# Kernel tuning notes

Hardware: AMD Instinct MI355X
Metric: run time of the kernel (lower is better)

## Reference

```python
import jax, jax.numpy as jnp
import numpy as np

B, N_PER, C, KG, KTOP, KNN = 8, 2048, 256, 16, 512, 32
N = B * N_PER
E = N * KG
EPS = 1e-5


def setup_inputs() -> dict:
    key = jax.random.key(0)
    ks = jax.random.split(key, 32)
    s = 0.05
    x = jax.random.normal(ks[0], (N, C), jnp.float32)
    x_origin = jax.random.normal(ks[1], (N, C), jnp.float32)
    xyz = jax.random.uniform(ks[2], (N, 3), jnp.float32)
    # graph: every node is a dst with KG incoming edges from random nodes of the SAME sample
    edge_dst = jnp.repeat(jnp.arange(N, dtype=jnp.int32), KG)
    src_local = jax.random.randint(ks[3], (E,), 0, N_PER, dtype=jnp.int32)
    edge_src = src_local + (edge_dst // N_PER) * N_PER
    # EdgeConv params (theta on x_j - x_i, phi on x_i)
    theta_w = jax.random.normal(ks[4], (C, C), jnp.float32) * s
    theta_b = jax.random.normal(ks[5], (C,), jnp.float32) * s
    phi_w = jax.random.normal(ks[6], (C, C), jnp.float32) * s
    phi_b = jax.random.normal(ks[7], (C,), jnp.float32) * s
    # region_score_mlp: Conv1d(C,64,1)-ReLU-BN(64)-Conv1d(64,32,1)-ReLU-BN(32)-Conv1d(32,1,1)
    w1 = jax.random.normal(ks[8], (64, C), jnp.float32) * s
    b1 = jax.random.normal(ks[9], (64,), jnp.float32) * s
    g1 = 1.0 + 0.1 * jax.random.normal(ks[10], (64,), jnp.float32)
    be1 = 0.1 * jax.random.normal(ks[11], (64,), jnp.float32)
    m1 = 0.1 * jax.random.normal(ks[12], (64,), jnp.float32)
    v1 = jax.random.uniform(ks[13], (64,), jnp.float32, 0.5, 1.5)
    w2 = jax.random.normal(ks[14], (32, 64), jnp.float32) * s
    b2 = jax.random.normal(ks[15], (32,), jnp.float32) * s
    g2 = 1.0 + 0.1 * jax.random.normal(ks[16], (32,), jnp.float32)
    be2 = 0.1 * jax.random.normal(ks[17], (32,), jnp.float32)
    m2 = 0.1 * jax.random.normal(ks[18], (32,), jnp.float32)
    v2 = jax.random.uniform(ks[19], (32,), jnp.float32, 0.5, 1.5)
    w3 = jax.random.normal(ks[20], (1, 32), jnp.float32) * s
    b3 = jax.random.normal(ks[21], (1,), jnp.float32) * s
    return dict(x=x, x_origin=x_origin, xyz=xyz, edge_src=edge_src, edge_dst=edge_dst,
                theta_w=theta_w, theta_b=theta_b, phi_w=phi_w, phi_b=phi_b,
                w1=w1, b1=b1, g1=g1, be1=be1, m1=m1, v1=v1,
                w2=w2, b2=b2, g2=g2, be2=be2, m2=m2, v2=v2, w3=w3, b3=b3)


def _bn(t, g, b, m, v):
    return (t - m) * jax.lax.rsqrt(v + EPS) * g + b


def _forward(x, x_origin, xyz, edge_src, edge_dst,
             theta_w, theta_b, phi_w, phi_b,
             w1, b1, g1, be1, m1, v1, w2, b2, g2, be2, m2, v2, w3, b3):
    # EdgeConv: h_i = max_{j->i}( theta(x_j - x_i) + phi(x_i) ), then residual add
    msg = ((x[edge_src] - x[edge_dst]) @ theta_w.T + theta_b
           + x[edge_dst] @ phi_w.T + phi_b)                      # [E, C]
    h = jax.ops.segment_max(msg, edge_dst, num_segments=N)       # [N, C]
    x1 = h + x                                                   # residual
    # per-node MLP (Conv1d kernel-size 1 == linear), BN in eval mode
    t = _bn(jax.nn.relu(x1 @ w1.T + b1), g1, be1, m1, v1)
    t = _bn(jax.nn.relu(t @ w2.T + b2), g2, be2, m2, v2)
    score = t @ w3.T + b3                                        # [N, 1]
    score_b = score.reshape(B, N_PER)                            # vps_score
    # per-batch top-k (cls=False path: select by raw score, descending)
    topk_vals, topk_idx = jax.lax.top_k(score_b, KTOP)           # [B, KTOP]
    perm = (topk_idx + jnp.arange(B, dtype=topk_idx.dtype)[:, None] * N_PER).reshape(-1)
    x_new = x1[perm].reshape(B, KTOP, C)
    x_copy = x_origin[perm].reshape(B, KTOP, -1)
    xyz_sel = xyz[perm].reshape(B, KTOP, 3)
    # rebuild 32-NN graph per sample on selected points (batched, no per-b python calls)
    d2 = jnp.sum((xyz_sel[:, :, None, :] - xyz_sel[:, None, :, :]) ** 2, axis=-1)  # [B,K,K]
    _, knn_idx = jax.lax.top_k(-d2, KNN)                         # [B, KTOP, 32]
    return knn_idx, x_new, x_copy, score_b, topk_vals


def reference(x, x_origin, xyz, edge_src, edge_dst,
              theta_w, theta_b, phi_w, phi_b,
              w1, b1, g1, be1, m1, v1, w2, b2, g2, be2, m2, v2, w3, b3):
    return _forward(x, x_origin, xyz, edge_src, edge_dst,
                    theta_w, theta_b, phi_w, phi_b,
                    w1, b1, g1, be1, m1, v1, w2, b2, g2, be2, m2, v2, w3, b3)
```

## Files before the change

### kernel.cpp

```cpp
#include <hip/hip_runtime.h>
#include <math.h>

constexpr int B     = 8;
constexpr int N_PER = 2048;
constexpr int C     = 256;
constexpr int KG    = 16;
constexpr int KTOP  = 512;
constexpr int KNN   = 32;
constexpr int N     = B * N_PER;
constexpr float EPS = 1e-5f;

__global__ __launch_bounds__(256, 2) void k1_dual_gemm(
    const float* __restrict__ x, const float* __restrict__ thw,
    const float* __restrict__ phw, const float* __restrict__ thb,
    const float* __restrict__ phb, float* __restrict__ T, float* __restrict__ R)
{
    constexpr int BK = 16, STX = 132, STW = 68;
    __shared__ float Xs[2][BK * STX];
    __shared__ float Wt[2][BK * STW];
    __shared__ float Wp[2][BK * STW];
    const int tid  = threadIdx.x;
    const int row0 = blockIdx.x * 128;
    const int n0   = blockIdx.y * 64;
    const int tx = tid & 15, ty = tid >> 4;
    const int lm = tid >> 1, lq = (tid & 1) * 8;
    const int wm = tid >> 2, wq = (tid & 3) * 4;

    float aT[8][4] = {{0.f}}, aQ[8][4] = {{0.f}};

    float4 nx0 = *(const float4*)(x   + (size_t)(row0 + lm) * C + lq);
    float4 nx1 = *(const float4*)(x   + (size_t)(row0 + lm) * C + lq + 4);
    float4 nt  = *(const float4*)(thw + (size_t)(n0   + wm) * C + wq);
    float4 np_ = *(const float4*)(phw + (size_t)(n0   + wm) * C + wq);
    Xs[0][(lq + 0) * STX + lm] = nx0.x;  Xs[0][(lq + 1) * STX + lm] = nx0.y;
    Xs[0][(lq + 2) * STX + lm] = nx0.z;  Xs[0][(lq + 3) * STX + lm] = nx0.w;
    Xs[0][(lq + 4) * STX + lm] = nx1.x;  Xs[0][(lq + 5) * STX + lm] = nx1.y;
    Xs[0][(lq + 6) * STX + lm] = nx1.z;  Xs[0][(lq + 7) * STX + lm] = nx1.w;
    Wt[0][(wq + 0) * STW + wm] = nt.x;   Wt[0][(wq + 1) * STW + wm] = nt.y;
    Wt[0][(wq + 2) * STW + wm] = nt.z;   Wt[0][(wq + 3) * STW + wm] = nt.w;
    Wp[0][(wq + 0) * STW + wm] = np_.x;  Wp[0][(wq + 1) * STW + wm] = np_.y;
    Wp[0][(wq + 2) * STW + wm] = np_.z;  Wp[0][(wq + 3) * STW + wm] = np_.w;
    __syncthreads();

    int p = 0;
    for (int k0 = 0; k0 < C; k0 += BK) {
        const int kn = k0 + BK;
        if (kn < C) {
            nx0 = *(const float4*)(x   + (size_t)(row0 + lm) * C + kn + lq);
            nx1 = *(const float4*)(x   + (size_t)(row0 + lm) * C + kn + lq + 4);
            nt  = *(const float4*)(thw + (size_t)(n0   + wm) * C + kn + wq);
            np_ = *(const float4*)(phw + (size_t)(n0   + wm) * C + kn + wq);
        }
        const float* Xp = Xs[p];
        const float* Tp = Wt[p];
        const float* Pp = Wp[p];
#pragma unroll
        for (int k = 0; k < BK; ++k) {
            float4 alo = *(const float4*)&Xp[k * STX + ty * 8];
            float4 ahi = *(const float4*)&Xp[k * STX + ty * 8 + 4];
            float4 tv4 = *(const float4*)&Tp[k * STW + tx * 4];
            float4 pv4 = *(const float4*)&Pp[k * STW + tx * 4];
            float av[8] = {alo.x, alo.y, alo.z, alo.w, ahi.x, ahi.y, ahi.z, ahi.w};
            float tv[4] = {tv4.x, tv4.y, tv4.z, tv4.w};
            float pv[4] = {pv4.x, pv4.y, pv4.z, pv4.w};
#pragma unroll
            for (int i2 = 0; i2 < 8; ++i2)
#pragma unroll
                for (int j2 = 0; j2 < 4; ++j2) {
                    aT[i2][j2] += av[i2] * tv[j2];
                    aQ[i2][j2] += av[i2] * pv[j2];
                }
        }
        if (kn < C) {
            const int q = p ^ 1;
            Xs[q][(lq + 0) * STX + lm] = nx0.x;  Xs[q][(lq + 1) * STX + lm] = nx0.y;
            Xs[q][(lq + 2) * STX + lm] = nx0.z;  Xs[q][(lq + 3) * STX + lm] = nx0.w;
            Xs[q][(lq + 4) * STX + lm] = nx1.x;  Xs[q][(lq + 5) * STX + lm] = nx1.y;
            Xs[q][(lq + 6) * STX + lm] = nx1.z;  Xs[q][(lq + 7) * STX + lm] = nx1.w;
            Wt[q][(wq + 0) * STW + wm] = nt.x;   Wt[q][(wq + 1) * STW + wm] = nt.y;
            Wt[q][(wq + 2) * STW + wm] = nt.z;   Wt[q][(wq + 3) * STW + wm] = nt.w;
            Wp[q][(wq + 0) * STW + wm] = np_.x;  Wp[q][(wq + 1) * STW + wm] = np_.y;
            Wp[q][(wq + 2) * STW + wm] = np_.z;  Wp[q][(wq + 3) * STW + wm] = np_.w;
            __syncthreads();
        }
        p ^= 1;
    }

    const int gn = n0 + tx * 4;
    const float4 tb4 = *(const float4*)(thb + gn);
    const float4 pb4 = *(const float4*)(phb + gn);
#pragma unroll
    for (int i2 = 0; i2 < 8; ++i2) {
        const int gm = row0 + ty * 8 + i2;
        const size_t off = (size_t)gm * C + gn;
        float4 xr = *(const float4*)(x + off);
        float4 tvv = make_float4(aT[i2][0], aT[i2][1], aT[i2][2], aT[i2][3]);
        float4 rv;
        rv.x = xr.x + aQ[i2][0] + tb4.x + pb4.x - tvv.x;
        rv.y = xr.y + aQ[i2][1] + tb4.y + pb4.y - tvv.y;
        rv.z = xr.z + aQ[i2][2] + tb4.z + pb4.z - tvv.z;
        rv.w = xr.w + aQ[i2][3] + tb4.w + pb4.w - tvv.w;
        *(float4*)(T + off) = tvv;
        *(float4*)(R + off) = rv;
    }
}

__global__ __launch_bounds__(256) void k2a_gather_max(
    const int* __restrict__ esrc, const float* __restrict__ T, float* x1r)
{
    const int gb = blockIdx.x;
    const int b  = gb & 7;
    const int node0 = b * N_PER + (gb >> 3) * 4;
    const int t = threadIdx.x;
    __shared__ int s[4][KG];
    if (t < 64) s[t >> 4][t & 15] = esrc[(node0 + (t >> 4)) * KG + (t & 15)];
    __syncthreads();
    const int m  = t >> 6;
    const int c4 = (t & 63) * 4;
    float4 acc = make_float4(-INFINITY, -INFINITY, -INFINITY, -INFINITY);
#pragma unroll
    for (int k = 0; k < KG; ++k) {
        const float4 v = *(const float4*)&T[(size_t)s[m][k] * C + c4];
        acc.x = fmaxf(acc.x, v.x);  acc.y = fmaxf(acc.y, v.y);
        acc.z = fmaxf(acc.z, v.z);  acc.w = fmaxf(acc.w, v.w);
    }
    const size_t off = (size_t)(node0 + m) * C + c4;
    float4 r = *(const float4*)&x1r[off];
    r.x += acc.x;  r.y += acc.y;  r.z += acc.z;  r.w += acc.w;
    *(float4*)&x1r[off] = r;
}

__global__ __launch_bounds__(256) void k2bc_score(
    const float* __restrict__ x1, const float* __restrict__ w1,
    const float* __restrict__ b1, const float* __restrict__ g1,
    const float* __restrict__ be1, const float* __restrict__ m1,
    const float* __restrict__ v1,
    const float* __restrict__ w2, const float* __restrict__ b2,
    const float* __restrict__ g2, const float* __restrict__ be2,
    const float* __restrict__ m2, const float* __restrict__ v2,
    const float* __restrict__ w3, const float* __restrict__ b3,
    float* __restrict__ score_ws, float* __restrict__ out_score)
{
    constexpr int BK = 16, ST = 68;
    __shared__ float Xs[BK * ST];
    __shared__ float Ws[BK * ST];
    __shared__ float t1s[64 * 65];
    __shared__ float w2s[32 * 65];
    __shared__ float w3s[32];
    __shared__ float zs[64 * 33];
    const int tid  = threadIdx.x;
    const int row0 = blockIdx.x * 64;
    const int tx = tid & 15, ty = tid >> 4;
    const int lm = tid >> 2, lq = (tid & 3) << 2;

    float acc[4][4] = {{0.f}};
    for (int k0 = 0; k0 < C; k0 += BK) {
        float4 fx = *(const float4*)(x1 + (size_t)(row0 + lm) * C + k0 + lq);
        float4 fw = *(const float4*)(w1 + (size_t)lm * C + k0 + lq);
        __syncthreads();
        Xs[(lq + 0) * ST + lm] = fx.x;  Xs[(lq + 1) * ST + lm] = fx.y;
        Xs[(lq + 2) * ST + lm] = fx.z;  Xs[(lq + 3) * ST + lm] = fx.w;
        Ws[(lq + 0) * ST + lm] = fw.x;  Ws[(lq + 1) * ST + lm] = fw.y;
        Ws[(lq + 2) * ST + lm] = fw.z;  Ws[(lq + 3) * ST + lm] = fw.w;
        __syncthreads();
#pragma unroll
        for (int k = 0; k < BK; ++k) {
            float4 a4 = *(const float4*)&Xs[k * ST + (ty << 2)];
            float4 w4 = *(const float4*)&Ws[k * ST + (tx << 2)];
            float av[4] = {a4.x, a4.y, a4.z, a4.w};
            float wv[4] = {w4.x, w4.y, w4.z, w4.w};
#pragma unroll
            for (int i2 = 0; i2 < 4; ++i2)
#pragma unroll
                for (int j2 = 0; j2 < 4; ++j2) acc[i2][j2] += av[i2] * wv[j2];
        }
    }
    __syncthreads();
#pragma unroll
    for (int i2 = 0; i2 < 4; ++i2) {
        const int mrow = (ty << 2) + i2;
#pragma unroll
        for (int j2 = 0; j2 < 4; ++j2) {
            const int o = (tx << 2) + j2;
            float y = acc[i2][j2] + b1[o];
            y = fmaxf(y, 0.f);
            y = (y - m1[o]) * (1.0f / sqrtf(v1[o] + EPS)) * g1[o] + be1[o];
            t1s[mrow * 65 + o] = y;
        }
    }
    for (int idx = tid; idx < 2048; idx += 256)
        w2s[(idx >> 6) * 65 + (idx & 63)] = w2[idx];
    if (tid < 32) w3s[tid] = w3[tid];
    __syncthreads();

    const int o = tid & 31;
    const float inv2 = (1.0f / sqrtf(v2[o] + EPS)) * g2[o];
#pragma unroll
    for (int p = 0; p < 8; ++p) {
        const int nl = p * 8 + (tid >> 5);
        float z = 0.f;
#pragma unroll
        for (int j = 0; j < 64; ++j) z += t1s[nl * 65 + j] * w2s[o * 65 + j];
        z += b2[o];
        z = fmaxf(z, 0.f);
        z = (z - m2[o]) * inv2 + be2[o];
        zs[nl * 33 + o] = z;
    }
    __syncthreads();

    if (tid < 64) {
        float sacc = 0.f;
#pragma unroll
        for (int j = 0; j < 32; ++j) sacc += zs[tid * 33 + j] * w3s[j];
        sacc += b3[0];
        const int node = row0 + tid;
        score_ws[node]  = sacc;
        out_score[node] = sacc;
    }
}

__global__ __launch_bounds__(1024) void k3_topk(
    const float* __restrict__ score, const float* __restrict__ xyz,
    float* __restrict__ out_topk, int* __restrict__ perm,
    float* __restrict__ xsel)
{
    __shared__ unsigned long long keys[N_PER];
    const int b = blockIdx.x;
    const int t = threadIdx.x;
    for (int i = t; i < N_PER; i += 1024) {
        const float v = score[b * N_PER + i];
        unsigned u = __float_as_uint(v);
        const unsigned ua = (u & 0x80000000u) ? ~u : (u | 0x80000000u);
        const unsigned ud = ~ua;
        keys[i] = ((unsigned long long)ud << 32) | (unsigned)i;
    }
    __syncthreads();
    for (int k = 2; k <= N_PER; k <<= 1) {
        for (int j = k >> 1; j > 0; j >>= 1) {
            for (int i = t; i < N_PER; i += 1024) {
                const int ixj = i ^ j;
                if (ixj > i) {
                    const unsigned long long a = keys[i], c = keys[ixj];
                    const bool up = ((i & k) == 0);
                    if ((a > c) == up) { keys[i] = c; keys[ixj] = a; }
                }
            }
            __syncthreads();
        }
    }
    for (int r = t; r < KTOP; r += 1024) {
        const int idx = (int)(keys[r] & 0xffffffffu);
        const int g = b * N_PER + idx;
        out_topk[b * KTOP + r] = score[g];
        perm[b * KTOP + r] = g;
        xsel[(b * KTOP + r) * 3 + 0] = xyz[g * 3 + 0];
        xsel[(b * KTOP + r) * 3 + 1] = xyz[g * 3 + 1];
        xsel[(b * KTOP + r) * 3 + 2] = xyz[g * 3 + 2];
    }
}

__global__ __launch_bounds__(256) void k5_knn(
    const int* __restrict__ perm, const float* __restrict__ xsel,
    const float* __restrict__ x1, const float* __restrict__ xorig,
    float* __restrict__ out_xnew, float* __restrict__ out_xcopy,
    float* __restrict__ out_knn)
{
    constexpr int G = 4;
    __shared__ float px[KTOP], py[KTOP], pz[KTOP];
    __shared__ unsigned long long keys[G * KTOP];
    const int t  = threadIdx.x;
    const int q0 = blockIdx.x * G;
    const int b  = q0 >> 9;
    const int i0 = q0 & 511;

    for (int idx = t; idx < KTOP; idx += 256) {
        const size_t base = ((size_t)b * KTOP + idx) * 3;
        px[idx] = xsel[base + 0];
        py[idx] = xsel[base + 1];
        pz[idx] = xsel[base + 2];
    }
#pragma unroll
    for (int p = 0; p < G; ++p) {
        const int row = q0 + p;
        const int g = perm[row];
        out_xnew [(size_t)row * C + t] = x1   [(size_t)g * C + t];
        out_xcopy[(size_t)row * C + t] = xorig[(size_t)g * C + t];
    }
    __syncthreads();

    for (int w = t; w < G * KTOP; w += 256) {
        const int p = w >> 9, idx = w & 511;
        const float dx = __fsub_rn(px[i0 + p], px[idx]);
        const float dy = __fsub_rn(py[i0 + p], py[idx]);
        const float dz = __fsub_rn(pz[i0 + p], pz[idx]);
        const float d2 = __fadd_rn(__fadd_rn(__fmul_rn(dx, dx), __fmul_rn(dy, dy)),
                                   __fmul_rn(dz, dz));
        keys[w] = ((unsigned long long)__float_as_uint(d2) << 32) | (unsigned)idx;
    }
    __syncthreads();

    for (int k = 2; k <= 32; k <<= 1) {
        for (int j = k >> 1; j > 0; j >>= 1) {
            for (int i = t; i < G * KTOP; i += 256) {
                const int ixj = i ^ j;
                if (ixj > i) {
                    const int il = i & 31;
                    const unsigned long long a = keys[i], c = keys[ixj];
                    const bool up = ((il & k) == 0) || (k == 32);
                    if ((a > c) == up) { keys[i] = c; keys[ixj] = a; }
                }
            }
            __syncthreads();
        }
    }
    for (int r = 0; r < 4; ++r) {
        const int npairs = 8 >> r;
        const int total  = G * npairs * 32;
        for (int w = t; w < total; w += 256) {
            const int p  = w / (npairs * 32);
            const int rm = w - p * (npairs * 32);
            const int m  = rm >> 5, i = rm & 31;
            const int baseA = p * KTOP + m * (64 << r);
            const int baseB = baseA + (32 << r);
            const unsigned long long a = keys[baseA + i];
            const unsigned long long c = keys[baseB + 31 - i];
            keys[baseA + i] = (c < a) ? c : a;
        }
        __syncthreads();
        for (int j = 16; j > 0; j >>= 1) {
            for (int w = t; w < total; w += 256) {
                const int p  = w / (npairs * 32);
                const int rm = w - p * (npairs * 32);
                const int m  = rm >> 5, i = rm & 31;
                const int ixj = i ^ j;
                if (ixj > i) {
                    const int baseA = p * KTOP + m * (64 << r);
                    const unsigned long long a = keys[baseA + i], c = keys[baseA + ixj];
                    if (a > c) { keys[baseA + i] = c; keys[baseA + ixj] = a; }
                }
            }
            __syncthreads();
        }
    }

    if (t < G * KNN) {
        const int p = t >> 5, r = t & 31;
        out_knn[((size_t)(q0 + p)) * KNN + r] =
            (float)(unsigned)(keys[p * KTOP + r] & 0xffffffffu);
    }
}

extern "C" void kernel_launch(void* const* d_in, const int* in_sizes, int n_in,
                              void* d_out, int out_size, void* d_ws, size_t ws_size,
                              hipStream_t stream)
{
    const float* x     = (const float*)d_in[0];
    const float* xorig = (const float*)d_in[1];
    const float* xyz   = (const float*)d_in[2];
    const int*   esrc  = (const int*)d_in[3];
    const float* thw = (const float*)d_in[5];
    const float* thb = (const float*)d_in[6];
    const float* phw = (const float*)d_in[7];
    const float* phb = (const float*)d_in[8];
    const float* w1  = (const float*)d_in[9];
    const float* b1  = (const float*)d_in[10];
    const float* g1  = (const float*)d_in[11];
    const float* be1 = (const float*)d_in[12];
    const float* m1  = (const float*)d_in[13];
    const float* v1  = (const float*)d_in[14];
    const float* w2  = (const float*)d_in[15];
    const float* b2  = (const float*)d_in[16];
    const float* g2  = (const float*)d_in[17];
    const float* be2 = (const float*)d_in[18];
    const float* m2  = (const float*)d_in[19];
    const float* v2  = (const float*)d_in[20];
    const float* w3  = (const float*)d_in[21];
    const float* b3  = (const float*)d_in[22];

    float* ws   = (float*)d_ws;
    float* T    = ws;
    float* x1   = ws + (size_t)N * C;
    float* sc   = ws + 2 * (size_t)N * C;
    int*   perm = (int*)(sc + N);
    float* xsel = (float*)(perm + B * KTOP);

    float* out     = (float*)d_out;
    float* o_knn   = out;
    float* o_xnew  = o_knn + (size_t)B * KTOP * KNN;
    float* o_xcopy = o_xnew + (size_t)B * KTOP * C;
    float* o_score = o_xcopy + (size_t)B * KTOP * C;
    float* o_topk  = o_score + (size_t)B * N_PER;

    k1_dual_gemm<<<dim3(N / 128, C / 64), 256, 0, stream>>>(x, thw, phw, thb, phb, T, x1);
    k2a_gather_max<<<N / 4, 256, 0, stream>>>(esrc, T, x1);
    k2bc_score<<<N / 64, 256, 0, stream>>>(x1, w1, b1, g1, be1, m1, v1,
                                           w2, b2, g2, be2, m2, v2, w3, b3, sc, o_score);
    k3_topk<<<B, 1024, 0, stream>>>(sc, xyz, o_topk, perm, xsel);
    k5_knn<<<B * KTOP / 4, 256, 0, stream>>>(perm, xsel, x1, xorig,
                                             o_xnew, o_xcopy, o_knn);
}
```

Measured before the change: 266.5 us.

## Widen GEMM K-tile, hold w2 in registers, and double k5 queries per block

The dual GEMM K-tile goes from 16 to 32, so each thread loads more per stage and the kernel hits half as many barriers, at the cost of more shared memory and registers per block. The score kernel now keeps its w2 row in registers and reads t1 with float4 loads, which drops the w2 shared buffer. The kNN kernel handles 8 query rows per block instead of 4 and copies the gathered rows with float4 loads and stores. The larger shared footprint in k1 and k5 may lower occupancy.

New measurement: 308.4 us. +15.7%, slower.

```diff
diff --git a/kernel.cpp b/kernel.cpp
--- a/kernel.cpp
+++ b/kernel.cpp
@@ -15,7 +15,7 @@
     const float* __restrict__ phw, const float* __restrict__ thb,
     const float* __restrict__ phb, float* __restrict__ T, float* __restrict__ R)
 {
-    constexpr int BK = 16, STX = 132, STW = 68;
+    constexpr int BK = 32, STX = 132, STW = 68;
     __shared__ float Xs[2][BK * STX];
     __shared__ float Wt[2][BK * STW];
     __shared__ float Wp[2][BK * STW];
@@ -23,33 +23,47 @@
     const int row0 = blockIdx.x * 128;
     const int n0   = blockIdx.y * 64;
     const int tx = tid & 15, ty = tid >> 4;
-    const int lm = tid >> 1, lq = (tid & 1) * 8;
-    const int wm = tid >> 2, wq = (tid & 3) * 4;
+    const int lm = tid >> 1, lq = (tid & 1) * 16;
+    const int wm = tid >> 2, wq = (tid & 3) * 8;
 
     float aT[8][4] = {{0.f}}, aQ[8][4] = {{0.f}};
 
-    float4 nx0 = *(const float4*)(x   + (size_t)(row0 + lm) * C + lq);
-    float4 nx1 = *(const float4*)(x   + (size_t)(row0 + lm) * C + lq + 4);
-    float4 nt  = *(const float4*)(thw + (size_t)(n0   + wm) * C + wq);
-    float4 np_ = *(const float4*)(phw + (size_t)(n0   + wm) * C + wq);
-    Xs[0][(lq + 0) * STX + lm] = nx0.x;  Xs[0][(lq + 1) * STX + lm] = nx0.y;
-    Xs[0][(lq + 2) * STX + lm] = nx0.z;  Xs[0][(lq + 3) * STX + lm] = nx0.w;
-    Xs[0][(lq + 4) * STX + lm] = nx1.x;  Xs[0][(lq + 5) * STX + lm] = nx1.y;
-    Xs[0][(lq + 6) * STX + lm] = nx1.z;  Xs[0][(lq + 7) * STX + lm] = nx1.w;
-    Wt[0][(wq + 0) * STW + wm] = nt.x;   Wt[0][(wq + 1) * STW + wm] = nt.y;
-    Wt[0][(wq + 2) * STW + wm] = nt.z;   Wt[0][(wq + 3) * STW + wm] = nt.w;
-    Wp[0][(wq + 0) * STW + wm] = np_.x;  Wp[0][(wq + 1) * STW + wm] = np_.y;
-    Wp[0][(wq + 2) * STW + wm] = np_.z;  Wp[0][(wq + 3) * STW + wm] = np_.w;
+    float4 nx0, nx1, nx2, nx3, nt0, nt1, np0, np1;
+    {
+        const float* xp = x   + (size_t)(row0 + lm) * C + lq;
+        const float* tp = thw + (size_t)(n0   + wm) * C + wq;
+        const float* pp = phw + (size_t)(n0   + wm) * C + wq;
+        nx0 = *(const float4*)(xp + 0);  nx1 = *(const float4*)(xp + 4);
+        nx2 = *(const float4*)(xp + 8);  nx3 = *(const float4*)(xp + 12);
+        nt0 = *(const float4*)(tp + 0);  nt1 = *(const float4*)(tp + 4);
+        np0 = *(const float4*)(pp + 0);  np1 = *(const float4*)(pp + 4);
+    }
+    {
+        float xs[16] = {nx0.x,nx0.y,nx0.z,nx0.w, nx1.x,nx1.y,nx1.z,nx1.w,
+                        nx2.x,nx2.y,nx2.z,nx2.w, nx3.x,nx3.y,nx3.z,nx3.w};
+        float ts[8]  = {nt0.x,nt0.y,nt0.z,nt0.w, nt1.x,nt1.y,nt1.z,nt1.w};
+        float ps[8]  = {np0.x,np0.y,np0.z,np0.w, np1.x,np1.y,np1.z,np1.w};
+#pragma unroll
+        for (int j = 0; j < 16; ++j) Xs[0][(lq + j) * STX + lm] = xs[j];
+#pragma unroll
+        for (int j = 0; j < 8; ++j) {
+            Wt[0][(wq + j) * STW + wm] = ts[j];
+            Wp[0][(wq + j) * STW + wm] = ps[j];
+        }
+    }
     __syncthreads();
 
     int p = 0;
     for (int k0 = 0; k0 < C; k0 += BK) {
         const int kn = k0 + BK;
         if (kn < C) {
-            nx0 = *(const float4*)(x   + (size_t)(row0 + lm) * C + kn + lq);
-            nx1 = *(const float4*)(x   + (size_t)(row0 + lm) * C + kn + lq + 4);
-            nt  = *(const float4*)(thw + (size_t)(n0   + wm) * C + kn + wq);
-            np_ = *(const float4*)(phw + (size_t)(n0   + wm) * C + kn + wq);
+            const float* xp = x   + (size_t)(row0 + lm) * C + kn + lq;
+            const float* tp = thw + (size_t)(n0   + wm) * C + kn + wq;
+            const float* pp = phw + (size_t)(n0   + wm) * C + kn + wq;
+            nx0 = *(const float4*)(xp + 0);  nx1 = *(const float4*)(xp + 4);
+            nx2 = *(const float4*)(xp + 8);  nx3 = *(const float4*)(xp + 12);
+            nt0 = *(const float4*)(tp + 0);  nt1 = *(const float4*)(tp + 4);
+            np0 = *(const float4*)(pp + 0);  np1 = *(const float4*)(pp + 4);
         }
         const float* Xp = Xs[p];
         const float* Tp = Wt[p];
@@ -73,14 +87,17 @@
         }
         if (kn < C) {
             const int q = p ^ 1;
-            Xs[q][(lq + 0) * STX + lm] = nx0.x;  Xs[q][(lq + 1) * STX + lm] = nx0.y;
-            Xs[q][(lq + 2) * STX + lm] = nx0.z;  Xs[q][(lq + 3) * STX + lm] = nx0.w;
-            Xs[q][(lq + 4) * STX + lm] = nx1.x;  Xs[q][(lq + 5) * STX + lm] = nx1.y;
-            Xs[q][(lq + 6) * STX + lm] = nx1.z;  Xs[q][(lq + 7) * STX + lm] = nx1.w;
-            Wt[q][(wq + 0) * STW + wm] = nt.x;   Wt[q][(wq + 1) * STW + wm] = nt.y;
-            Wt[q][(wq + 2) * STW + wm] = nt.z;   Wt[q][(wq + 3) * STW + wm] = nt.w;
-            Wp[q][(wq + 0) * STW + wm] = np_.x;  Wp[q][(wq + 1) * STW + wm] = np_.y;
-            Wp[q][(wq + 2) * STW + wm] = np_.z;  Wp[q][(wq + 3) * STW + wm] = np_.w;
+            float xs[16] = {nx0.x,nx0.y,nx0.z,nx0.w, nx1.x,nx1.y,nx1.z,nx1.w,
+                            nx2.x,nx2.y,nx2.z,nx2.w, nx3.x,nx3.y,nx3.z,nx3.w};
+            float ts[8]  = {nt0.x,nt0.y,nt0.z,nt0.w, nt1.x,nt1.y,nt1.z,nt1.w};
+            float ps[8]  = {np0.x,np0.y,np0.z,np0.w, np1.x,np1.y,np1.z,np1.w};
+#pragma unroll
+            for (int j = 0; j < 16; ++j) Xs[q][(lq + j) * STX + lm] = xs[j];
+#pragma unroll
+            for (int j = 0; j < 8; ++j) {
+                Wt[q][(wq + j) * STW + wm] = ts[j];
+                Wp[q][(wq + j) * STW + wm] = ps[j];
+            }
             __syncthreads();
         }
         p ^= 1;
@@ -93,7 +110,7 @@
     for (int i2 = 0; i2 < 8; ++i2) {
         const int gm = row0 + ty * 8 + i2;
         const size_t off = (size_t)gm * C + gn;
-        float4 xr = *(const float4*)(x + off);
+        const float4 xr = *(const float4*)(x + off);
         float4 tvv = make_float4(aT[i2][0], aT[i2][1], aT[i2][2], aT[i2][3]);
         float4 rv;
         rv.x = xr.x + aQ[i2][0] + tb4.x + pb4.x - tvv.x;
@@ -141,17 +158,23 @@
     const float* __restrict__ w3, const float* __restrict__ b3,
     float* __restrict__ score_ws, float* __restrict__ out_score)
 {
-    constexpr int BK = 16, ST = 68;
+    constexpr int BK = 16, ST = 68, T1ST = 68;
     __shared__ float Xs[BK * ST];
     __shared__ float Ws[BK * ST];
-    __shared__ float t1s[64 * 65];
-    __shared__ float w2s[32 * 65];
+    __shared__ float t1s[64 * T1ST];
     __shared__ float w3s[32];
     __shared__ float zs[64 * 33];
     const int tid  = threadIdx.x;
     const int row0 = blockIdx.x * 64;
     const int tx = tid & 15, ty = tid >> 4;
     const int lm = tid >> 2, lq = (tid & 3) << 2;
+    const int o  = tid & 31;
+
+    float4 w2r[16];
+#pragma unroll
+    for (int j4 = 0; j4 < 16; ++j4)
+        w2r[j4] = *(const float4*)&w2[o * 64 + j4 * 4];
+    if (tid < 32) w3s[tid] = w3[tid];
 
     float acc[4][4] = {{0.f}};
     for (int k0 = 0; k0 < C; k0 += BK) {
@@ -181,26 +204,28 @@
         const int mrow = (ty << 2) + i2;
 #pragma unroll
         for (int j2 = 0; j2 < 4; ++j2) {
-            const int o = (tx << 2) + j2;
-            float y = acc[i2][j2] + b1[o];
+            const int oc = (tx << 2) + j2;
+            float y = acc[i2][j2] + b1[oc];
             y = fmaxf(y, 0.f);
-            y = (y - m1[o]) * (1.0f / sqrtf(v1[o] + EPS)) * g1[o] + be1[o];
-            t1s[mrow * 65 + o] = y;
-        }
-    }
-    for (int idx = tid; idx < 2048; idx += 256)
-        w2s[(idx >> 6) * 65 + (idx & 63)] = w2[idx];
-    if (tid < 32) w3s[tid] = w3[tid];
-    __syncthreads();
-
-    const int o = tid & 31;
+            y = (y - m1[oc]) * (1.0f / sqrtf(v1[oc] + EPS)) * g1[oc] + be1[oc];
+            t1s[mrow * T1ST + oc] = y;
+        }
+    }
+    __syncthreads();
+
     const float inv2 = (1.0f / sqrtf(v2[o] + EPS)) * g2[o];
 #pragma unroll
     for (int p = 0; p < 8; ++p) {
         const int nl = p * 8 + (tid >> 5);
         float z = 0.f;
 #pragma unroll
-        for (int j = 0; j < 64; ++j) z += t1s[nl * 65 + j] * w2s[o * 65 + j];
+        for (int j4 = 0; j4 < 16; ++j4) {
+            const float4 tv = *(const float4*)&t1s[nl * T1ST + j4 * 4];
+            z += tv.x * w2r[j4].x;
+            z += tv.y * w2r[j4].y;
+            z += tv.z * w2r[j4].z;
+            z += tv.w * w2r[j4].w;
+        }
         z += b2[o];
         z = fmaxf(z, 0.f);
         z = (z - m2[o]) * inv2 + be2[o];
@@ -265,7 +290,7 @@
     float* __restrict__ out_xnew, float* __restrict__ out_xcopy,
     float* __restrict__ out_knn)
 {
-    constexpr int G = 4;
+    constexpr int G = 8;
     __shared__ float px[KTOP], py[KTOP], pz[KTOP];
     __shared__ unsigned long long keys[G * KTOP];
     const int t  = threadIdx.x;
@@ -279,12 +304,16 @@
         py[idx] = xsel[base + 1];
         pz[idx] = xsel[base + 2];
     }
-#pragma unroll
-    for (int p = 0; p < G; ++p) {
-        const int row = q0 + p;
+    {
+        const int pr = t >> 5;
+        const int row = q0 + pr;
         const int g = perm[row];
-        out_xnew [(size_t)row * C + t] = x1   [(size_t)g * C + t];
-        out_xcopy[(size_t)row * C + t] = xorig[(size_t)g * C + t];
+#pragma unroll
+        for (int h = 0; h < 2; ++h) {
+            const int c4 = (t & 31) * 4 + h * 128;
+            *(float4*)&out_xnew [(size_t)row * C + c4] = *(const float4*)&x1   [(size_t)g * C + c4];
+            *(float4*)&out_xcopy[(size_t)row * C + c4] = *(const float4*)&xorig[(size_t)g * C + c4];
+        }
     }
     __syncthreads();
 
@@ -343,7 +372,7 @@
         }
     }
 
-    if (t < G * KNN) {
+    {
         const int p = t >> 5, r = t & 31;
         out_knn[((size_t)(q0 + p)) * KNN + r] =
             (float)(unsigned)(keys[p * KTOP + r] & 0xffffffffu);
@@ -396,6 +425,6 @@
     k2bc_score<<<N / 64, 256, 0, stream>>>(x1, w1, b1, g1, be1, m1, v1,
                                            w2, b2, g2, be2, m2, v2, w3, b3, sc, o_score);
     k3_topk<<<B, 1024, 0, stream>>>(sc, xyz, o_topk, perm, xsel);
-    k5_knn<<<B * KTOP / 4, 256, 0, stream>>>(perm, xsel, x1, xorig,
+    k5_knn<<<B * KTOP / 8, 256, 0, stream>>>(perm, xsel, x1, xorig,
                                              o_xnew, o_xcopy, o_knn);
 }
```

## Shrink score tiles, keep w2 in registers, drop intra-wave barriers in sorts

Applied to the files above, without the earlier changes.

The score kernel now processes 32 rows per block instead of 64, doubling the block count, and holds w2 rows in registers, reading t1 with float4 loads. The bitonic sorts in the top-k and kNN kernels skip __syncthreads for stages whose compare partners sit in the same 64-wide wavefront, using volatile shared memory instead. The kNN kernel handles 8 queries per block and copies gathered rows with float4. This cuts barrier count and gives more parallelism in the score MLP, but relies on lockstep wavefront execution for correctness.

Result: slower. 337.3 us (+26.6%).

```diff
diff --git a/kernel.cpp b/kernel.cpp
--- a/kernel.cpp
+++ b/kernel.cpp
@@ -93,7 +93,7 @@
     for (int i2 = 0; i2 < 8; ++i2) {
         const int gm = row0 + ty * 8 + i2;
         const size_t off = (size_t)gm * C + gn;
-        float4 xr = *(const float4*)(x + off);
+        const float4 xr = *(const float4*)(x + off);
         float4 tvv = make_float4(aT[i2][0], aT[i2][1], aT[i2][2], aT[i2][3]);
         float4 rv;
         rv.x = xr.x + aQ[i2][0] + tb4.x + pb4.x - tvv.x;
@@ -141,66 +141,77 @@
     const float* __restrict__ w3, const float* __restrict__ b3,
     float* __restrict__ score_ws, float* __restrict__ out_score)
 {
-    constexpr int BK = 16, ST = 68;
+    constexpr int BK = 16, ST = 68, T1ST = 68;
     __shared__ float Xs[BK * ST];
     __shared__ float Ws[BK * ST];
-    __shared__ float t1s[64 * 65];
-    __shared__ float w2s[32 * 65];
+    __shared__ float t1s[32 * T1ST];
     __shared__ float w3s[32];
-    __shared__ float zs[64 * 33];
+    __shared__ float zs[32 * 33];
     const int tid  = threadIdx.x;
-    const int row0 = blockIdx.x * 64;
+    const int row0 = blockIdx.x * 32;
     const int tx = tid & 15, ty = tid >> 4;
-    const int lm = tid >> 2, lq = (tid & 3) << 2;
-
-    float acc[4][4] = {{0.f}};
+    const int o  = tid & 31;
+
+    float4 w2r[16];
+#pragma unroll
+    for (int j4 = 0; j4 < 16; ++j4)
+        w2r[j4] = *(const float4*)&w2[o * 64 + j4 * 4];
+    if (tid < 32) w3s[tid] = w3[tid];
+
+    const int xr = tid >> 2, xq = (tid & 3) * 4;
+    float acc[2][4] = {{0.f}};
     for (int k0 = 0; k0 < C; k0 += BK) {
-        float4 fx = *(const float4*)(x1 + (size_t)(row0 + lm) * C + k0 + lq);
-        float4 fw = *(const float4*)(w1 + (size_t)lm * C + k0 + lq);
+        float4 fx;
+        if (tid < 128) fx = *(const float4*)(x1 + (size_t)(row0 + xr) * C + k0 + xq);
+        float4 fw = *(const float4*)(w1 + (size_t)xr * C + k0 + xq);
         __syncthreads();
-        Xs[(lq + 0) * ST + lm] = fx.x;  Xs[(lq + 1) * ST + lm] = fx.y;
-        Xs[(lq + 2) * ST + lm] = fx.z;  Xs[(lq + 3) * ST + lm] = fx.w;
-        Ws[(lq + 0) * ST + lm] = fw.x;  Ws[(lq + 1) * ST + lm] = fw.y;
-        Ws[(lq + 2) * ST + lm] = fw.z;  Ws[(lq + 3) * ST + lm] = fw.w;
+        if (tid < 128) {
+            Xs[(xq + 0) * ST + xr] = fx.x;  Xs[(xq + 1) * ST + xr] = fx.y;
+            Xs[(xq + 2) * ST + xr] = fx.z;  Xs[(xq + 3) * ST + xr] = fx.w;
+        }
+        Ws[(xq + 0) * ST + xr] = fw.x;  Ws[(xq + 1) * ST + xr] = fw.y;
+        Ws[(xq + 2) * ST + xr] = fw.z;  Ws[(xq + 3) * ST + xr] = fw.w;
         __syncthreads();
 #pragma unroll
         for (int k = 0; k < BK; ++k) {
-            float4 a4 = *(const float4*)&Xs[k * ST + (ty << 2)];
-            float4 w4 = *(const float4*)&Ws[k * ST + (tx << 2)];
-            float av[4] = {a4.x, a4.y, a4.z, a4.w};
+            const float2 a2 = *(const float2*)&Xs[k * ST + ty * 2];
+            const float4 w4 = *(const float4*)&Ws[k * ST + tx * 4];
+            float av[2] = {a2.x, a2.y};
             float wv[4] = {w4.x, w4.y, w4.z, w4.w};
 #pragma unroll
-            for (int i2 = 0; i2 < 4; ++i2)
+            for (int i2 = 0; i2 < 2; ++i2)
 #pragma unroll
                 for (int j2 = 0; j2 < 4; ++j2) acc[i2][j2] += av[i2] * wv[j2];
         }
     }
     __syncthreads();
 #pragma unroll
-    for (int i2 = 0; i2 < 4; ++i2) {
-        const int mrow = (ty << 2) + i2;
+    for (int i2 = 0; i2 < 2; ++i2) {
+        const int mrow = ty * 2 + i2;
 #pragma unroll
         for (int j2 = 0; j2 < 4; ++j2) {
-            const int o = (tx << 2) + j2;
-            float y = acc[i2][j2] + b1[o];
+            const int oc = tx * 4 + j2;
+            float y = acc[i2][j2] + b1[oc];
             y = fmaxf(y, 0.f);
-            y = (y - m1[o]) * (1.0f / sqrtf(v1[o] + EPS)) * g1[o] + be1[o];
-            t1s[mrow * 65 + o] = y;
-        }
-    }
-    for (int idx = tid; idx < 2048; idx += 256)
-        w2s[(idx >> 6) * 65 + (idx & 63)] = w2[idx];
-    if (tid < 32) w3s[tid] = w3[tid];
-    __syncthreads();
-
-    const int o = tid & 31;
+            y = (y - m1[oc]) * (1.0f / sqrtf(v1[oc] + EPS)) * g1[oc] + be1[oc];
+            t1s[mrow * T1ST + oc] = y;
+        }
+    }
+    __syncthreads();
+
     const float inv2 = (1.0f / sqrtf(v2[o] + EPS)) * g2[o];
 #pragma unroll
-    for (int p = 0; p < 8; ++p) {
+    for (int p = 0; p < 4; ++p) {
         const int nl = p * 8 + (tid >> 5);
         float z = 0.f;
 #pragma unroll
-        for (int j = 0; j < 64; ++j) z += t1s[nl * 65 + j] * w2s[o * 65 + j];
+        for (int j4 = 0; j4 < 16; ++j4) {
+            const float4 tv = *(const float4*)&t1s[nl * T1ST + j4 * 4];
+            z += tv.x * w2r[j4].x;
+            z += tv.y * w2r[j4].y;
+            z += tv.z * w2r[j4].z;
+            z += tv.w * w2r[j4].w;
+        }
         z += b2[o];
         z = fmaxf(z, 0.f);
         z = (z - m2[o]) * inv2 + be2[o];
@@ -208,7 +219,7 @@
     }
     __syncthreads();
 
-    if (tid < 64) {
+    if (tid < 32) {
         float sacc = 0.f;
 #pragma unroll
         for (int j = 0; j < 32; ++j) sacc += zs[tid * 33 + j] * w3s[j];
@@ -225,6 +236,7 @@
     float* __restrict__ xsel)
 {
     __shared__ unsigned long long keys[N_PER];
+    volatile unsigned long long* vk = keys;
     const int b = blockIdx.x;
     const int t = threadIdx.x;
     for (int i = t; i < N_PER; i += 1024) {
@@ -234,20 +246,23 @@
         const unsigned ud = ~ua;
         keys[i] = ((unsigned long long)ud << 32) | (unsigned)i;
     }
-    __syncthreads();
+    bool need_bar = true;
     for (int k = 2; k <= N_PER; k <<= 1) {
         for (int j = k >> 1; j > 0; j >>= 1) {
+            const bool cross = (j >= 64);
+            if (cross || need_bar) __syncthreads();
             for (int i = t; i < N_PER; i += 1024) {
                 const int ixj = i ^ j;
                 if (ixj > i) {
-                    const unsigned long long a = keys[i], c = keys[ixj];
+                    const unsigned long long a = vk[i], c = vk[ixj];
                     const bool up = ((i & k) == 0);
-                    if ((a > c) == up) { keys[i] = c; keys[ixj] = a; }
+                    if ((a > c) == up) { vk[i] = c; vk[ixj] = a; }
                 }
             }
-            __syncthreads();
-        }
-    }
+            need_bar = cross;
+        }
+    }
+    __syncthreads();
     for (int r = t; r < KTOP; r += 1024) {
         const int idx = (int)(keys[r] & 0xffffffffu);
         const int g = b * N_PER + idx;
@@ -265,9 +280,10 @@
     float* __restrict__ out_xnew, float* __restrict__ out_xcopy,
     float* __restrict__ out_knn)
 {
-    constexpr int G = 4;
+    constexpr int G = 8;
     __shared__ float px[KTOP], py[KTOP], pz[KTOP];
     __shared__ unsigned long long keys[G * KTOP];
+    volatile unsigned long long* vk = keys;
     const int t  = threadIdx.x;
     const int q0 = blockIdx.x * G;
     const int b  = q0 >> 9;
@@ -279,12 +295,16 @@
         py[idx] = xsel[base + 1];
         pz[idx] = xsel[base + 2];
     }
-#pragma unroll
-    for (int p = 0; p < G; ++p) {
-        const int row = q0 + p;
+    {
+        const int pr = t >> 5;
+        const int row = q0 + pr;
         const int g = perm[row];
-        out_xnew [(size_t)row * C + t] = x1   [(size_t)g * C + t];
-        out_xcopy[(size_t)row * C + t] = xorig[(size_t)g * C + t];
+#pragma unroll
+        for (int h = 0; h < 2; ++h) {
+            const int c4 = (t & 31) * 4 + h * 128;
+            *(float4*)&out_xnew [(size_t)row * C + c4] = *(const float4*)&x1   [(size_t)g * C + c4];
+            *(float4*)&out_xcopy[(size_t)row * C + c4] = *(const float4*)&xorig[(size_t)g * C + c4];
+        }
     }
     __syncthreads();
 
@@ -297,7 +317,6 @@
                                    __fmul_rn(dz, dz));
         keys[w] = ((unsigned long long)__float_as_uint(d2) << 32) | (unsigned)idx;
     }
-    __syncthreads();
 
     for (int k = 2; k <= 32; k <<= 1) {
         for (int j = k >> 1; j > 0; j >>= 1) {
@@ -305,28 +324,28 @@
                 const int ixj = i ^ j;
                 if (ixj > i) {
                     const int il = i & 31;
-                    const unsigned long long a = keys[i], c = keys[ixj];
+                    const unsigned long long a = vk[i], c = vk[ixj];
                     const bool up = ((il & k) == 0) || (k == 32);
-                    if ((a > c) == up) { keys[i] = c; keys[ixj] = a; }
+                    if ((a > c) == up) { vk[i] = c; vk[ixj] = a; }
                 }
             }
-            __syncthreads();
-        }
-    }
+        }
+    }
+
     for (int r = 0; r < 4; ++r) {
         const int npairs = 8 >> r;
         const int total  = G * npairs * 32;
+        __syncthreads();
         for (int w = t; w < total; w += 256) {
             const int p  = w / (npairs * 32);
             const int rm = w - p * (npairs * 32);
             const int m  = rm >> 5, i = rm & 31;
             const int baseA = p * KTOP + m * (64 << r);
             const int baseB = baseA + (32 << r);
-            const unsigned long long a = keys[baseA + i];
-            const unsigned long long c = keys[baseB + 31 - i];
-            keys[baseA + i] = (c < a) ? c : a;
-        }
-        __syncthreads();
+            const unsigned long long a = vk[baseA + i];
+            const unsigned long long c = vk[baseB + 31 - i];
+            vk[baseA + i] = (c < a) ? c : a;
+        }
         for (int j = 16; j > 0; j >>= 1) {
             for (int w = t; w < total; w += 256) {
                 const int p  = w / (npairs * 32);
@@ -335,15 +354,15 @@
                 const int ixj = i ^ j;
                 if (ixj > i) {
                     const int baseA = p * KTOP + m * (64 << r);
-                    const unsigned long long a = keys[baseA + i], c = keys[baseA + ixj];
-                    if (a > c) { keys[baseA + i] = c; keys[baseA + ixj] = a; }
+                    const unsigned long long a = vk[baseA + i], c = vk[baseA + ixj];
+                    if (a > c) { vk[baseA + i] = c; vk[baseA + ixj] = a; }
                 }
             }
-            __syncthreads();
-        }
-    }
-
-    if (t < G * KNN) {
+        }
+    }
+    __syncthreads();
+
+    {
         const int p = t >> 5, r = t & 31;
         out_knn[((size_t)(q0 + p)) * KNN + r] =
             (float)(unsigned)(keys[p * KTOP + r] & 0xffffffffu);
@@ -393,9 +412,9 @@
 
     k1_dual_gemm<<<dim3(N / 128, C / 64), 256, 0, stream>>>(x, thw, phw, thb, phb, T, x1);
     k2a_gather_max<<<N / 4, 256, 0, stream>>>(esrc, T, x1);
-    k2bc_score<<<N / 64, 256, 0, stream>>>(x1, w1, b1, g1, be1, m1, v1,
+    k2bc_score<<<N / 32, 256, 0, stream>>>(x1, w1, b1, g1, be1, m1, v1,
                                            w2, b2, g2, be2, m2, v2, w3, b3, sc, o_score);
     k3_topk<<<B, 1024, 0, stream>>>(sc, xyz, o_topk, perm, xsel);
-    k5_knn<<<B * KTOP / 4, 256, 0, stream>>>(perm, xsel, x1, xorig,
+    k5_knn<<<B * KTOP / 8, 256, 0, stream>>>(perm, xsel, x1, xorig,
                                              o_xnew, o_xcopy, o_knn);
 }
```

## Remap GEMM blocks per batch, register-cache w2, and widen knn query groups

Applied to the files above, without the earlier changes.

The dual GEMM and score kernels now map a flat block index so that consecutive blocks interleave across batches, which may spread the work differently across XCDs and caches. In the score kernel, the w2 weights move from shared memory into per-thread float4 registers, and the t1 tile is read with float4 loads. The knn kernel handles 8 query rows per block instead of 4, and the x_new/x_copy row copies become vectorised float4 loads and stores. Larger register use and a doubled shared keys buffer may reduce occupancy.

Result: no change. 271.3 us (+1.8%).

```diff
diff --git a/kernel.cpp b/kernel.cpp
--- a/kernel.cpp
+++ b/kernel.cpp
@@ -19,9 +19,12 @@
     __shared__ float Xs[2][BK * STX];
     __shared__ float Wt[2][BK * STW];
     __shared__ float Wp[2][BK * STW];
+    const int f     = blockIdx.x;
+    const int batch = f & 7;
+    const int jj    = f >> 3;
+    const int row0  = (batch * 16 + (jj & 15)) * 128;
+    const int n0    = (jj >> 4) * 64;
     const int tid  = threadIdx.x;
-    const int row0 = blockIdx.x * 128;
-    const int n0   = blockIdx.y * 64;
     const int tx = tid & 15, ty = tid >> 4;
     const int lm = tid >> 1, lq = (tid & 1) * 8;
     const int wm = tid >> 2, wq = (tid & 3) * 4;
@@ -93,7 +96,7 @@
     for (int i2 = 0; i2 < 8; ++i2) {
         const int gm = row0 + ty * 8 + i2;
         const size_t off = (size_t)gm * C + gn;
-        float4 xr = *(const float4*)(x + off);
+        const float4 xr = *(const float4*)(x + off);
         float4 tvv = make_float4(aT[i2][0], aT[i2][1], aT[i2][2], aT[i2][3]);
         float4 rv;
         rv.x = xr.x + aQ[i2][0] + tb4.x + pb4.x - tvv.x;
@@ -141,17 +144,24 @@
     const float* __restrict__ w3, const float* __restrict__ b3,
     float* __restrict__ score_ws, float* __restrict__ out_score)
 {
-    constexpr int BK = 16, ST = 68;
+    constexpr int BK = 16, ST = 68, T1ST = 68;
     __shared__ float Xs[BK * ST];
     __shared__ float Ws[BK * ST];
-    __shared__ float t1s[64 * 65];
-    __shared__ float w2s[32 * 65];
+    __shared__ float t1s[64 * T1ST];
     __shared__ float w3s[32];
     __shared__ float zs[64 * 33];
     const int tid  = threadIdx.x;
-    const int row0 = blockIdx.x * 64;
+    const int f    = blockIdx.x;
+    const int row0 = (f & 7) * N_PER + (f >> 3) * 64;
     const int tx = tid & 15, ty = tid >> 4;
     const int lm = tid >> 2, lq = (tid & 3) << 2;
+    const int o  = tid & 31;
+
+    float4 w2r[16];
+#pragma unroll
+    for (int j4 = 0; j4 < 16; ++j4)
+        w2r[j4] = *(const float4*)&w2[o * 64 + j4 * 4];
+    if (tid < 32) w3s[tid] = w3[tid];
 
     float acc[4][4] = {{0.f}};
     for (int k0 = 0; k0 < C; k0 += BK) {
@@ -181,26 +191,28 @@
         const int mrow = (ty << 2) + i2;
 #pragma unroll
         for (int j2 = 0; j2 < 4; ++j2) {
-            const int o = (tx << 2) + j2;
-            float y = acc[i2][j2] + b1[o];
+            const int oc = (tx << 2) + j2;
+            float y = acc[i2][j2] + b1[oc];
             y = fmaxf(y, 0.f);
-            y = (y - m1[o]) * (1.0f / sqrtf(v1[o] + EPS)) * g1[o] + be1[o];
-            t1s[mrow * 65 + o] = y;
-        }
-    }
-    for (int idx = tid; idx < 2048; idx += 256)
-        w2s[(idx >> 6) * 65 + (idx & 63)] = w2[idx];
-    if (tid < 32) w3s[tid] = w3[tid];
-    __syncthreads();
-
-    const int o = tid & 31;
+            y = (y - m1[oc]) * (1.0f / sqrtf(v1[oc] + EPS)) * g1[oc] + be1[oc];
+            t1s[mrow * T1ST + oc] = y;
+        }
+    }
+    __syncthreads();
+
     const float inv2 = (1.0f / sqrtf(v2[o] + EPS)) * g2[o];
 #pragma unroll
     for (int p = 0; p < 8; ++p) {
         const int nl = p * 8 + (tid >> 5);
         float z = 0.f;
 #pragma unroll
-        for (int j = 0; j < 64; ++j) z += t1s[nl * 65 + j] * w2s[o * 65 + j];
+        for (int j4 = 0; j4 < 16; ++j4) {
+            const float4 tv = *(const float4*)&t1s[nl * T1ST + j4 * 4];
+            z += tv.x * w2r[j4].x;
+            z += tv.y * w2r[j4].y;
+            z += tv.z * w2r[j4].z;
+            z += tv.w * w2r[j4].w;
+        }
         z += b2[o];
         z = fmaxf(z, 0.f);
         z = (z - m2[o]) * inv2 + be2[o];
@@ -265,7 +277,7 @@
     float* __restrict__ out_xnew, float* __restrict__ out_xcopy,
     float* __restrict__ out_knn)
 {
-    constexpr int G = 4;
+    constexpr int G = 8;
     __shared__ float px[KTOP], py[KTOP], pz[KTOP];
     __shared__ unsigned long long keys[G * KTOP];
     const int t  = threadIdx.x;
@@ -279,12 +291,16 @@
         py[idx] = xsel[base + 1];
         pz[idx] = xsel[base + 2];
     }
-#pragma unroll
-    for (int p = 0; p < G; ++p) {
-        const int row = q0 + p;
+    {
+        const int pr = t >> 5;
+        const int row = q0 + pr;
         const int g = perm[row];
-        out_xnew [(size_t)row * C + t] = x1   [(size_t)g * C + t];
-        out_xcopy[(size_t)row * C + t] = xorig[(size_t)g * C + t];
+#pragma unroll
+        for (int h = 0; h < 2; ++h) {
+            const int c4 = (t & 31) * 4 + h * 128;
+            *(float4*)&out_xnew [(size_t)row * C + c4] = *(const float4*)&x1   [(size_t)g * C + c4];
+            *(float4*)&out_xcopy[(size_t)row * C + c4] = *(const float4*)&xorig[(size_t)g * C + c4];
+        }
     }
     __syncthreads();
 
@@ -343,7 +359,7 @@
         }
     }
 
-    if (t < G * KNN) {
+    {
         const int p = t >> 5, r = t & 31;
         out_knn[((size_t)(q0 + p)) * KNN + r] =
             (float)(unsigned)(keys[p * KTOP + r] & 0xffffffffu);
@@ -391,11 +407,11 @@
     float* o_score = o_xcopy + (size_t)B * KTOP * C;
     float* o_topk  = o_score + (size_t)B * N_PER;
 
-    k1_dual_gemm<<<dim3(N / 128, C / 64), 256, 0, stream>>>(x, thw, phw, thb, phb, T, x1);
+    k1_dual_gemm<<<512, 256, 0, stream>>>(x, thw, phw, thb, phb, T, x1);
     k2a_gather_max<<<N / 4, 256, 0, stream>>>(esrc, T, x1);
     k2bc_score<<<N / 64, 256, 0, stream>>>(x1, w1, b1, g1, be1, m1, v1,
                                            w2, b2, g2, be2, m2, v2, w3, b3, sc, o_score);
     k3_topk<<<B, 1024, 0, stream>>>(sc, xyz, o_topk, perm, xsel);
-    k5_knn<<<B * KTOP / 4, 256, 0, stream>>>(perm, xsel, x1, xorig,
+    k5_knn<<<B * KTOP / 8, 256, 0, stream>>>(perm, xsel, x1, xorig,
                                              o_xnew, o_xcopy, o_knn);
 }
```
